# Optimization experiments

Hardware: AMD Instinct MI355X
Metric: run time of the kernel (lower is better)

Reference implementation:

```python
import jax, jax.numpy as jnp
import numpy as np


def setup_inputs() -> dict:
    key = jax.random.key(0)
    k1, k2 = jax.random.split(key)
    B, F, E = 16384, 200, 64
    features = jax.random.normal(k1, (B, F), dtype=jnp.float32)
    # per-feature Linear(1, E, bias=False) weights, stacked: [F, E]
    W = jax.random.uniform(k2, (F, E), dtype=jnp.float32, minval=-1e-4, maxval=1e-4)
    return {"features": features, "W": W}


def reference(features, W):
    # emb[b, f, e] = features[b, f] * W[f, e]  (rank-1 'Linear(1,E)' per feature)
    # sum over features then square:  (sum_f f_bf * W_fe)^2 = (features @ W)^2
    sum_emb = jnp.einsum('bf,fe->be', features, W)            # [B, E]
    # sum over features of squares: sum_f (f_bf * W_fe)^2 = (features^2) @ (W^2)
    sq_sum = jnp.einsum('bf,fe->be', features * features, W * W)  # [B, E]
    # FM second-order term, summed over embedding dim, keepdim
    predicts = jnp.sum(sum_emb * sum_emb - sq_sum, axis=1, keepdims=True)  # [B, 1]
    return predicts
```

## Files before the change

kernel.cpp:

```cpp
#include <hip/hip_runtime.h>


constexpr int F  = 200;
constexpr int RB = 64;
constexpr int KP = 232;
constexpr float WSCALE = 8192.0f;
constexpr float OSCALE = 1.0f / (WSCALE * WSCALE);

typedef _Float16 half8 __attribute__((ext_vector_type(8)));
typedef _Float16 half4 __attribute__((ext_vector_type(4)));
typedef float floatx4 __attribute__((ext_vector_type(4)));

__global__ __launch_bounds__(256)
void fm_v6(const float* __restrict__ X, const float* __restrict__ W,
           float* __restrict__ out)
{
    __shared__ alignas(16) _Float16 wt[64][KP];
    __shared__ alignas(16) _Float16 xt[RB][KP];
    __shared__ alignas(16) float    sf[F];
    __shared__ alignas(16) float    res[RB];

    const int t    = threadIdx.x;
    const int lane = t & 63;
    const int w    = __builtin_amdgcn_readfirstlane(t >> 6);
    const int rowBase = (int)blockIdx.x * RB;

    const int r = t >> 2, sub = t & 3;
    const floatx4* Xr = (const floatx4*)(X + (size_t)(rowBase + r) * F);
    floatx4 xv[13];
    #pragma unroll
    for (int j = 0; j < 13; ++j) {
        int f4 = sub + 4 * j;
        if (f4 < 50) xv[j] = Xr[f4];
    }

    {
        const floatx4* W4 = (const floatx4*)W;
        for (int j = 0; j < 13; ++j) {
            int i = t + 256 * j;
            if (i < 3200) {
                floatx4 w4 = W4[i];
                int f  = i >> 4;
                int e0 = (i & 15) * 4;
                float ss = w4.x*w4.x + w4.y*w4.y + w4.z*w4.z + w4.w*w4.w;
                ss += __shfl_xor(ss, 1, 64);
                ss += __shfl_xor(ss, 2, 64);
                ss += __shfl_xor(ss, 4, 64);
                ss += __shfl_xor(ss, 8, 64);
                if ((t & 15) == 0) sf[f] = ss;
                wt[e0 + 0][f] = (_Float16)(w4.x * WSCALE);
                wt[e0 + 1][f] = (_Float16)(w4.y * WSCALE);
                wt[e0 + 2][f] = (_Float16)(w4.z * WSCALE);
                wt[e0 + 3][f] = (_Float16)(w4.w * WSCALE);
            }
        }
        half8 z = {};
        *(half8*)&wt[t >> 2][200 + 8 * (t & 3)] = z;
        *(half8*)&xt[t >> 2][200 + 8 * (t & 3)] = z;
    }

    #pragma unroll
    for (int j = 0; j < 13; ++j) {
        int f4 = sub + 4 * j;
        if (f4 < 50) {
            floatx4 x4 = xv[j];
            half4 h;
            h[0] = (_Float16)x4.x; h[1] = (_Float16)x4.y;
            h[2] = (_Float16)x4.z; h[3] = (_Float16)x4.w;
            *(half4*)&xt[r][4 * f4] = h;
        }
    }
    __syncthreads();

    {
        float q = 0.f;
        #pragma unroll
        for (int j = 0; j < 13; ++j) {
            int f4 = sub + 4 * j;
            if (f4 < 50) {
                floatx4 x4 = xv[j];
                floatx4 s4 = *(const floatx4*)&sf[4 * f4];
                q += x4.x*x4.x*s4.x + x4.y*x4.y*s4.y + x4.z*x4.z*s4.z + x4.w*x4.w*s4.w;
            }
        }
        q += __shfl_xor(q, 1, 64);
        q += __shfl_xor(q, 2, 64);
        if (sub == 0) res[r] = -q;
    }

    const int lm = lane & 15, lq = lane >> 4;
    floatx4 acc0 = {}, acc1 = {}, acc2 = {}, acc3 = {};
    {
        const half8* ap = (const half8*)&xt[16 * w + lm][lq * 8];
        const half8* b0 = (const half8*)&wt[ 0 + lm][lq * 8];
        const half8* b1 = (const half8*)&wt[16 + lm][lq * 8];
        const half8* b2 = (const half8*)&wt[32 + lm][lq * 8];
        const half8* b3 = (const half8*)&wt[48 + lm][lq * 8];
        #pragma unroll
        for (int kk = 0; kk < 7; ++kk) {
            half8 a = ap[kk * 4];
            acc0 = __builtin_amdgcn_mfma_f32_16x16x32_f16(a, b0[kk * 4], acc0, 0, 0, 0);
            acc1 = __builtin_amdgcn_mfma_f32_16x16x32_f16(a, b1[kk * 4], acc1, 0, 0, 0);
            acc2 = __builtin_amdgcn_mfma_f32_16x16x32_f16(a, b2[kk * 4], acc2, 0, 0, 0);
            acc3 = __builtin_amdgcn_mfma_f32_16x16x32_f16(a, b3[kk * 4], acc3, 0, 0, 0);
        }
    }
    __syncthreads();

    {
        float p[4];
        #pragma unroll
        for (int r2 = 0; r2 < 4; ++r2)
            p[r2] = acc0[r2]*acc0[r2] + acc1[r2]*acc1[r2]
                  + acc2[r2]*acc2[r2] + acc3[r2]*acc3[r2];
        #pragma unroll
        for (int r2 = 0; r2 < 4; ++r2) {
            p[r2] += __shfl_xor(p[r2], 1, 64);
            p[r2] += __shfl_xor(p[r2], 2, 64);
            p[r2] += __shfl_xor(p[r2], 4, 64);
            p[r2] += __shfl_xor(p[r2], 8, 64);
        }
        if (lm == 0) {
            #pragma unroll
            for (int r2 = 0; r2 < 4; ++r2) {
                int row = 16 * w + lq * 4 + r2;
                out[rowBase + row] = fmaf(p[r2], OSCALE, res[row]);
            }
        }
    }
}

extern "C" void kernel_launch(void* const* d_in, const int* in_sizes, int n_in,
                              void* d_out, int out_size, void* d_ws, size_t ws_size,
                              hipStream_t stream) {
    const float* X = (const float*)d_in[0];
    const float* W = (const float*)d_in[1];
    float* out = (float*)d_out;

    const int B = in_sizes[0] / F;
    fm_v6<<<B / RB, 256, 0, stream>>>(X, W, out);
}
```

Baseline: 67.16 us.

## Precompute fp16 weights in a prep kernel and stream X directly into MFMA

Splits the work into a small prep kernel that converts W to a padded fp16 transposed layout and the per-feature squared sums, stored in workspace, and a main kernel with 16 rows per block. Each wave computes one 16-column slice of E, loading X straight from global memory into MFMA operands with no LDS staging. This removes the per-block redundant conversion of W and the LDS round trip for X. In exchange, every X row is read by four waves instead of once, there is an extra kernel launch, and there are many more small blocks.

```diff
diff --git a/kernel.cpp b/kernel.cpp
--- a/kernel.cpp
+++ b/kernel.cpp
@@ -2,131 +2,103 @@
 
 
 constexpr int F  = 200;
-constexpr int RB = 64;
-constexpr int KP = 232;
+constexpr int KP = 224;
 constexpr float WSCALE = 8192.0f;
 constexpr float OSCALE = 1.0f / (WSCALE * WSCALE);
 
 typedef _Float16 half8 __attribute__((ext_vector_type(8)));
-typedef _Float16 half4 __attribute__((ext_vector_type(4)));
 typedef float floatx4 __attribute__((ext_vector_type(4)));
 
 __global__ __launch_bounds__(256)
-void fm_v6(const float* __restrict__ X, const float* __restrict__ W,
-           float* __restrict__ out)
+void fm_prep(const float* __restrict__ W, _Float16* __restrict__ wt,
+             float* __restrict__ sf)
 {
-    __shared__ alignas(16) _Float16 wt[64][KP];
-    __shared__ alignas(16) _Float16 xt[RB][KP];
-    __shared__ alignas(16) float    sf[F];
-    __shared__ alignas(16) float    res[RB];
+    const int t = threadIdx.x;
+    const int i = (int)blockIdx.x * 256 + t;
+    if (i < 3200) {
+        floatx4 w4 = ((const floatx4*)W)[i];
+        const int f  = i >> 4;
+        const int e0 = (i & 15) * 4;
+        float ss = w4.x*w4.x + w4.y*w4.y + w4.z*w4.z + w4.w*w4.w;
+        ss += __shfl_xor(ss, 1, 64);
+        ss += __shfl_xor(ss, 2, 64);
+        ss += __shfl_xor(ss, 4, 64);
+        ss += __shfl_xor(ss, 8, 64);
+        if ((t & 15) == 0) sf[f] = ss;
+        wt[(e0 + 0) * KP + f] = (_Float16)(w4.x * WSCALE);
+        wt[(e0 + 1) * KP + f] = (_Float16)(w4.y * WSCALE);
+        wt[(e0 + 2) * KP + f] = (_Float16)(w4.z * WSCALE);
+        wt[(e0 + 3) * KP + f] = (_Float16)(w4.w * WSCALE);
+    }
+    if (blockIdx.x == 12 && t >= 128) {
+        const int j = t - 128;
+        half8 z = {};
+        for (int c = j; c < 192; c += 128) {
+            int e = c / 3, part = c - 3 * e;
+            *(half8*)(wt + e * KP + 200 + part * 8) = z;
+        }
+        if (j < 24) sf[200 + j] = 0.f;
+    }
+}
+
+__global__ __launch_bounds__(256, 4)
+void fm_v7(const float* __restrict__ X, const _Float16* __restrict__ wt,
+           const float* __restrict__ sf, float* __restrict__ out)
+{
+    __shared__ float p_lds[4][16];
+    __shared__ float q_lds[16];
 
     const int t    = threadIdx.x;
     const int lane = t & 63;
     const int w    = __builtin_amdgcn_readfirstlane(t >> 6);
-    const int rowBase = (int)blockIdx.x * RB;
+    const int lm   = lane & 15, lq = lane >> 4;
+    const int row  = (int)blockIdx.x * 16 + lm;
 
-    const int r = t >> 2, sub = t & 3;
-    const floatx4* Xr = (const floatx4*)(X + (size_t)(rowBase + r) * F);
-    floatx4 xv[13];
+    const float*    xr = X + (size_t)row * F;
+    const _Float16* wr = wt + (16 * w + lm) * KP + lq * 8;
+
+    floatx4 acc = {};
+    float q = 0.f;
     #pragma unroll
-    for (int j = 0; j < 13; ++j) {
-        int f4 = sub + 4 * j;
-        if (f4 < 50) xv[j] = Xr[f4];
+    for (int kk = 0; kk < 7; ++kk) {
+        half8 a = *(const half8*)(wr + kk * 32);
+        half8 b;
+        if (kk < 6 || lq == 0) {
+            const int k0 = kk * 32 + lq * 8;
+            floatx4 x0 = *(const floatx4*)(xr + k0);
+            floatx4 x1 = *(const floatx4*)(xr + k0 + 4);
+            if (w == 0) {
+                floatx4 s0 = *(const floatx4*)(sf + k0);
+                floatx4 s1 = *(const floatx4*)(sf + k0 + 4);
+                q += x0.x*x0.x*s0.x + x0.y*x0.y*s0.y + x0.z*x0.z*s0.z + x0.w*x0.w*s0.w
+                   + x1.x*x1.x*s1.x + x1.y*x1.y*s1.y + x1.z*x1.z*s1.z + x1.w*x1.w*s1.w;
+            }
+            b[0] = (_Float16)x0.x; b[1] = (_Float16)x0.y;
+            b[2] = (_Float16)x0.z; b[3] = (_Float16)x0.w;
+            b[4] = (_Float16)x1.x; b[5] = (_Float16)x1.y;
+            b[6] = (_Float16)x1.z; b[7] = (_Float16)x1.w;
+        } else {
+            b = (half8){};
+        }
+        acc = __builtin_amdgcn_mfma_f32_16x16x32_f16(a, b, acc, 0, 0, 0);
     }
 
-    {
-        const floatx4* W4 = (const floatx4*)W;
-        for (int j = 0; j < 13; ++j) {
-            int i = t + 256 * j;
-            if (i < 3200) {
-                floatx4 w4 = W4[i];
-                int f  = i >> 4;
-                int e0 = (i & 15) * 4;
-                float ss = w4.x*w4.x + w4.y*w4.y + w4.z*w4.z + w4.w*w4.w;
-                ss += __shfl_xor(ss, 1, 64);
-                ss += __shfl_xor(ss, 2, 64);
-                ss += __shfl_xor(ss, 4, 64);
-                ss += __shfl_xor(ss, 8, 64);
-                if ((t & 15) == 0) sf[f] = ss;
-                wt[e0 + 0][f] = (_Float16)(w4.x * WSCALE);
-                wt[e0 + 1][f] = (_Float16)(w4.y * WSCALE);
-                wt[e0 + 2][f] = (_Float16)(w4.z * WSCALE);
-                wt[e0 + 3][f] = (_Float16)(w4.w * WSCALE);
-            }
-        }
-        half8 z = {};
-        *(half8*)&wt[t >> 2][200 + 8 * (t & 3)] = z;
-        *(half8*)&xt[t >> 2][200 + 8 * (t & 3)] = z;
+    float p = acc[0]*acc[0] + acc[1]*acc[1] + acc[2]*acc[2] + acc[3]*acc[3];
+    p += __shfl_xor(p, 16, 64);
+    p += __shfl_xor(p, 32, 64);
+    if (w == 0) {
+        q += __shfl_xor(q, 16, 64);
+        q += __shfl_xor(q, 32, 64);
     }
-
-    #pragma unroll
-    for (int j = 0; j < 13; ++j) {
-        int f4 = sub + 4 * j;
-        if (f4 < 50) {
-            floatx4 x4 = xv[j];
-            half4 h;
-            h[0] = (_Float16)x4.x; h[1] = (_Float16)x4.y;
-            h[2] = (_Float16)x4.z; h[3] = (_Float16)x4.w;
-            *(half4*)&xt[r][4 * f4] = h;
-        }
+    if (lq == 0) {
+        p_lds[w][lm] = p;
+        if (w == 0) q_lds[lm] = q;
     }
     __syncthreads();
-
-    {
-        float q = 0.f;
-        #pragma unroll
-        for (int j = 0; j < 13; ++j) {
-            int f4 = sub + 4 * j;
-            if (f4 < 50) {
-                floatx4 x4 = xv[j];
-                floatx4 s4 = *(const floatx4*)&sf[4 * f4];
-                q += x4.x*x4.x*s4.x + x4.y*x4.y*s4.y + x4.z*x4.z*s4.z + x4.w*x4.w*s4.w;
-            }
-        }
-        q += __shfl_xor(q, 1, 64);
-        q += __shfl_xor(q, 2, 64);
-        if (sub == 0) res[r] = -q;
-    }
-
-    const int lm = lane & 15, lq = lane >> 4;
-    floatx4 acc0 = {}, acc1 = {}, acc2 = {}, acc3 = {};
-    {
-        const half8* ap = (const half8*)&xt[16 * w + lm][lq * 8];
-        const half8* b0 = (const half8*)&wt[ 0 + lm][lq * 8];
-        const half8* b1 = (const half8*)&wt[16 + lm][lq * 8];
-        const half8* b2 = (const half8*)&wt[32 + lm][lq * 8];
-        const half8* b3 = (const half8*)&wt[48 + lm][lq * 8];
-        #pragma unroll
-        for (int kk = 0; kk < 7; ++kk) {
-            half8 a = ap[kk * 4];
-            acc0 = __builtin_amdgcn_mfma_f32_16x16x32_f16(a, b0[kk * 4], acc0, 0, 0, 0);
-            acc1 = __builtin_amdgcn_mfma_f32_16x16x32_f16(a, b1[kk * 4], acc1, 0, 0, 0);
-            acc2 = __builtin_amdgcn_mfma_f32_16x16x32_f16(a, b2[kk * 4], acc2, 0, 0, 0);
-            acc3 = __builtin_amdgcn_mfma_f32_16x16x32_f16(a, b3[kk * 4], acc3, 0, 0, 0);
-        }
-    }
-    __syncthreads();
-
-    {
-        float p[4];
-        #pragma unroll
-        for (int r2 = 0; r2 < 4; ++r2)
-            p[r2] = acc0[r2]*acc0[r2] + acc1[r2]*acc1[r2]
-                  + acc2[r2]*acc2[r2] + acc3[r2]*acc3[r2];
-        #pragma unroll
-        for (int r2 = 0; r2 < 4; ++r2) {
-            p[r2] += __shfl_xor(p[r2], 1, 64);
-            p[r2] += __shfl_xor(p[r2], 2, 64);
-            p[r2] += __shfl_xor(p[r2], 4, 64);
-            p[r2] += __shfl_xor(p[r2], 8, 64);
-        }
-        if (lm == 0) {
-            #pragma unroll
-            for (int r2 = 0; r2 < 4; ++r2) {
-                int row = 16 * w + lq * 4 + r2;
-                out[rowBase + row] = fmaf(p[r2], OSCALE, res[row]);
-            }
-        }
+    if (t < 16) {
+        float r = (p_lds[0][t] + p_lds[1][t] + p_lds[2][t] + p_lds[3][t]) * OSCALE
+                - q_lds[t];
+        out[(size_t)blockIdx.x * 16 + t] = r;
     }
 }
 
@@ -137,6 +109,10 @@
     const float* W = (const float*)d_in[1];
     float* out = (float*)d_out;
 
+    _Float16* wt = (_Float16*)d_ws;
+    float*    sf = (float*)((char*)d_ws + 64 * KP * sizeof(_Float16));
+
     const int B = in_sizes[0] / F;
-    fm_v6<<<B / RB, 256, 0, stream>>>(X, W, out);
+    fm_prep<<<13, 256, 0, stream>>>(W, wt, sf);
+    fm_v7<<<B / 16, 256, 0, stream>>>(X, wt, sf, out);
 }
```

New measurement: 67.13 us. About the same (-0.0%).
